# Optimization experiments

Measured on AMD Instinct MI355X. Metric: run time of the kernel, lower is better.

Reference implementation:

```python
import jax, jax.numpy as jnp
import numpy as np

B, LQ, LK, D = 8, 1024, 4096, 1024


def setup_inputs() -> dict:
    key = jax.random.key(0)
    k1, k2, k3, k4, k5, k6 = jax.random.split(key, 6)
    s = 1.0 / np.sqrt(D)
    return {
        "T": jax.random.normal(k1, (B, LQ, D), dtype=jnp.float32),
        "S": jax.random.normal(k2, (B, LK, D), dtype=jnp.float32),
        "Wq": jax.random.uniform(k3, (D, D), jnp.float32, -s, s),
        "Wk": jax.random.uniform(k4, (D, D), jnp.float32, -s, s),
        "Wv": jax.random.uniform(k5, (D, D), jnp.float32, -s, s),
        "Wo": jax.random.uniform(k6, (D, D), jnp.float32, -s, s),
    }


def reference(T, S, Wq, Wk, Wv, Wo):
    # Linear layers: y = x @ W.T (torch nn.Linear convention), bias=False
    q = jnp.einsum('bqd,ed->bqe', T, Wq)          # [B, LQ, D]
    k = jnp.einsum('bkd,ed->bke', S, Wk)          # [B, LK, D]
    v = jnp.einsum('bkd,ed->bke', S, Wv)          # [B, LK, D]
    scale = jnp.asarray(D, q.dtype) ** -0.5        # hidden_dim ** -0.5 (single head)
    attn = jnp.einsum('bqe,bke->bqk', q, k) * scale  # [B, LQ, LK]
    attn = jax.nn.softmax(attn, axis=-1)
    out = jnp.einsum('bqk,bke->bqe', attn, v)      # [B, LQ, D]
    return jnp.einsum('bqe,fe->bqf', out, Wo)      # output projection
```

## Files before the change

### kernel.cpp

```cpp
#include <hip/hip_runtime.h>
#include <stdint.h>

typedef __bf16 bf16;
typedef __bf16 bf16x8 __attribute__((ext_vector_type(8)));
typedef float f32x4 __attribute__((ext_vector_type(4)));

__device__ __forceinline__ void gload_lds16(const void* g, void* l) {
    __builtin_amdgcn_global_load_lds(
        (const __attribute__((address_space(1))) unsigned int*)g,
        (__attribute__((address_space(3))) unsigned int*)l, 16, 0, 0);
}

#define BAR()    asm volatile("s_barrier" ::: "memory")
#define WAITV(N) asm volatile("s_waitcnt vmcnt(" #N ")" ::: "memory")

template<int OMODE>
__global__ __launch_bounds__(512, 2)
void gemm256(const bf16* __restrict__ A, const bf16* __restrict__ B,
             void* __restrict__ Cv, int K, int N,
             long batchA, long batchB, long batchC, float alpha,
             int nbx, int nby, int GC, int lda, int ldb)
{
    __shared__ __align__(16) bf16 lds[2][4][8192];

    const int nwg  = gridDim.x;
    const int orig = blockIdx.x;
    const int q8   = nwg >> 3, r8 = nwg & 7;
    const int xcd  = orig & 7, lid = orig >> 3;
    const int p    = (xcd < r8 ? xcd * (q8 + 1) : r8 * (q8 + 1) + (xcd - r8) * q8) + lid;

    int pd = p, hv = 0;
    if constexpr (OMODE == 3) { hv = p >> 7; pd = p & 127; }
    const int kOff = hv << 11;

    const int perb = nbx * nby;
    const int z    = pd / perb;
    const int pb   = pd - z * perb;
    const int sw   = nby * GC;
    const int st   = pb / sw;
    const int rem  = pb - st * sw;
    const int by   = rem / GC;
    const int bx   = st * GC + (rem - by * GC);

    const long rowb = (long)by << 8;
    const long colb = (long)bx << 8;

    const int t  = threadIdx.x;
    const int l  = t & 63;
    const int w  = t >> 6;
    const int wm = w >> 2;
    const int wn = w & 3;

    const int sL   = (t * 16) ^ (((t >> 3) & 3) << 4);
    const int srow = sL >> 6;
    const int sk   = (sL & 63) >> 1;
    const bf16* gA = A + (long)z * batchA + (rowb + srow) * (long)lda + sk + kOff;
    const bf16* gB = B + (long)z * batchB + (colb + srow) * (long)ldb + sk + kOff;
    const long rA = 128L * lda;
    const long rB = 128L * ldb;
    const int  d0 = t * 8, d1 = t * 8 + 4096;

    const int xl    = ((l >> 1) & 3) << 4;
    const int aBase = ((wm * 128 + (l & 15)) * 64 + ((l >> 4) << 4)) ^ xl;
    const int bBase = ((wn * 64  + (l & 15)) * 64 + ((l >> 4) << 4)) ^ xl;

    f32x4 acc[8][4] = {};
    bf16x8 av[4], bv[4];

#define STG(S, R, G, KOFF2, RS) do { \
    const bf16* _g = (G) + (KOFF2); \
    gload_lds16(_g,      &lds[S][R][d0]); \
    gload_lds16(_g + RS, &lds[S][R][d1]); \
  } while (0)

#define RD(S, R, OFF) (*(const bf16x8*)((const char*)&lds[S][R][0] + (OFF)))

#define MM(MB) \
    __builtin_amdgcn_s_setprio(1); \
    _Pragma("unroll") for (int mi = 0; mi < 4; ++mi) \
      _Pragma("unroll") for (int nj = 0; nj < 4; ++nj) \
        acc[MB + mi][nj] = __builtin_amdgcn_mfma_f32_16x16x32_bf16(av[mi], bv[nj], acc[MB + mi][nj], 0, 0, 0); \
    __builtin_amdgcn_s_setprio(0);

#define PH1(S, STGX) { \
    _Pragma("unroll") for (int nj = 0; nj < 4; ++nj) bv[nj] = RD(S, 2, bBase + nj * 1024); \
    _Pragma("unroll") for (int mi = 0; mi < 4; ++mi) av[mi] = RD(S, 0, aBase + mi * 1024); \
    STGX; BAR(); MM(0) BAR(); }

#define PH2(S, STGX) { \
    _Pragma("unroll") for (int mi = 0; mi < 4; ++mi) av[mi] = RD(S, 0, aBase + 4096 + mi * 1024); \
    STGX; BAR(); MM(4) BAR(); }

#define PH3(S, STGX) { \
    _Pragma("unroll") for (int nj = 0; nj < 4; ++nj) bv[nj] = RD(S, 3, bBase + nj * 1024); \
    _Pragma("unroll") for (int mi = 0; mi < 4; ++mi) av[mi] = RD(S, 1, aBase + mi * 1024); \
    STGX; BAR(); MM(0) BAR(); }

#define PH4(S, STGX, WT) { \
    _Pragma("unroll") for (int mi = 0; mi < 4; ++mi) av[mi] = RD(S, 1, aBase + 4096 + mi * 1024); \
    STGX; BAR(); MM(4) WT; BAR(); }

    STG(0, 0, gA, 0,  rA);
    STG(0, 1, gA, 32, rA);
    STG(0, 2, gB, 0,  rB);
    STG(0, 3, gB, 32, rB);
    STG(1, 2, gB, 64, rB);
    STG(1, 0, gA, 64, rA);
    STG(1, 3, gB, 96, rB);
    WAITV(6);
    BAR();

    const int NI = K >> 7;
    for (int i = 0; i < NI - 1; ++i) {
        const int kb = i << 7;
        const int kn = kb + 128;
        PH1(0, STG(1, 1, gA, kb + 96, rA));
        PH2(0, STG(0, 2, gB, kn,      rB));
        PH3(0, STG(0, 0, gA, kn,      rA));
        PH4(0, STG(0, 3, gB, kn + 32, rB), WAITV(6));
        PH1(1, STG(0, 1, gA, kn + 32, rA));
        PH2(1, STG(1, 2, gB, kn + 64, rB));
        PH3(1, STG(1, 0, gA, kn + 64, rA));
        PH4(1, STG(1, 3, gB, kn + 96, rB), WAITV(6));
    }
    {
        const int kb = (NI - 1) << 7;
        PH1(0, STG(1, 1, gA, kb + 96, rA));
        PH2(0, );
        PH3(0, );
        PH4(0, , WAITV(0));
        PH1(1, );
        PH2(1, );
        PH3(1, );
        PH4(1, , );
    }
#undef STG
#undef RD
#undef MM
#undef PH1
#undef PH2
#undef PH3
#undef PH4

    const int r0 = (l >> 4) << 2;

    if constexpr (OMODE == 2) {
        const long cb0 = colb + wn * 64 + (l & 15);
        const long rb0 = rowb + wm * 128 + r0;
#pragma unroll
        for (int mf = 0; mf < 8; ++mf)
#pragma unroll
          for (int nj = 0; nj < 4; ++nj) {
            const long col = cb0 + nj * 16;
#pragma unroll
            for (int r = 0; r < 4; ++r) {
                const long row = rb0 + mf * 16 + r;
                ((float*)Cv)[(long)z * batchC + row * (long)N + col] = acc[mf][nj][r] * alpha;
            }
          }
    } else if constexpr (OMODE == 3) {
        float* Cb = (float*)Cv + (long)hv * 8388608 + (long)z * 1048576;
        const long cb0 = colb + wn * 64 + (l & 15);
        const long rb0 = rowb + wm * 128 + r0;
#pragma unroll
        for (int mf = 0; mf < 8; ++mf)
#pragma unroll
          for (int nj = 0; nj < 4; ++nj) {
            const long col = cb0 + nj * 16;
#pragma unroll
            for (int r = 0; r < 4; ++r)
                Cb[(rb0 + mf * 16 + r) * 1024 + col] = acc[mf][nj][r];
          }
    } else {
        bf16* epi = &lds[0][0][0];
        const int rrow   = t >> 5;
        const int cchunk = (t & 31) << 3;
        const int myh = (OMODE == 0) ? wm : (wn >> 1);
#pragma unroll
        for (int h = 0; h < 2; ++h) {
            if (myh == h) {
#pragma unroll
                for (int mf = 0; mf < 8; ++mf)
#pragma unroll
                  for (int nj = 0; nj < 4; ++nj)
#pragma unroll
                    for (int r = 0; r < 4; ++r) {
                        const float v = acc[mf][nj][r] * alpha;
                        int orow = wm * 128 + mf * 16 + r0 + r;
                        int ocol = wn * 64 + nj * 16 + (l & 15);
                        if (OMODE == 1) { int tmp = orow; orow = ocol; ocol = tmp; }
                        epi[(orow - h * 128) * 280 + ocol] = (bf16)v;
                    }
            }
            __syncthreads();
#pragma unroll
            for (int pp = 0; pp < 8; ++pp) {
                const int lrow = pp * 16 + rrow;
                const int row  = h * 128 + lrow;
                uint4 d = *(const uint4*)&epi[lrow * 280 + cchunk];
                if (OMODE == 0) {
                    bf16* Cb = (bf16*)Cv + (long)z * batchC;
                    *(uint4*)&Cb[(rowb + row) * (long)N + colb + cchunk] = d;
                } else {
                    const long zz  = rowb >> 12;
                    const long lk0 = (rowb & 4095) + cchunk;
                    *(uint4*)&((bf16*)Cv)[zz * 4194304L + (colb + row) * 4096L + lk0] = d;
                }
            }
            __syncthreads();
        }
    }
}

__global__ void cvt_bf16(const float* __restrict__ in, bf16* __restrict__ out, long n8)
{
    const long stride = (long)gridDim.x * 256;
    for (long i = (long)blockIdx.x * 256 + threadIdx.x; i < n8; i += stride) {
        const float4* p = (const float4*)in + i * 2;
        float4 a = p[0], b = p[1];
        union { bf16 h[8]; uint4 u; } o;
        o.h[0] = (bf16)a.x; o.h[1] = (bf16)a.y; o.h[2] = (bf16)a.z; o.h[3] = (bf16)a.w;
        o.h[4] = (bf16)b.x; o.h[5] = (bf16)b.y; o.h[6] = (bf16)b.z; o.h[7] = (bf16)b.w;
        ((uint4*)out)[i] = o.u;
    }
}

__global__ void cvt_w4(const float* __restrict__ wq, const float* __restrict__ wk,
                       const float* __restrict__ wv, const float* __restrict__ wo,
                       bf16* __restrict__ out)
{
    const long i  = (long)blockIdx.x * 256 + threadIdx.x;
    const int seg = (int)(i >> 17);
    const long j  = i & 131071;
    const float* src = seg == 0 ? wq : seg == 1 ? wk : seg == 2 ? wv : wo;
    const float4* pp = (const float4*)src + j * 2;
    float4 a = pp[0], b = pp[1];
    union { bf16 h[8]; uint4 u; } o;
    o.h[0] = (bf16)a.x; o.h[1] = (bf16)a.y; o.h[2] = (bf16)a.z; o.h[3] = (bf16)a.w;
    o.h[4] = (bf16)b.x; o.h[5] = (bf16)b.y; o.h[6] = (bf16)b.z; o.h[7] = (bf16)b.w;
    ((uint4*)out)[i] = o.u;
}

__global__ void reduce_pv(const float* __restrict__ Pt, bf16* __restrict__ Ob)
{
    const long i = (long)blockIdx.x * 256 + threadIdx.x;
    const float4* a = (const float4*)Pt + i * 2;
    const float4* b = (const float4*)(Pt + 8388608) + i * 2;
    float4 x0 = a[0], x1 = a[1], y0 = b[0], y1 = b[1];
    union { bf16 h[8]; uint4 u; } o;
    o.h[0] = (bf16)(x0.x + y0.x); o.h[1] = (bf16)(x0.y + y0.y);
    o.h[2] = (bf16)(x0.z + y0.z); o.h[3] = (bf16)(x0.w + y0.w);
    o.h[4] = (bf16)(x1.x + y1.x); o.h[5] = (bf16)(x1.y + y1.y);
    o.h[6] = (bf16)(x1.z + y1.z); o.h[7] = (bf16)(x1.w + y1.w);
    ((uint4*)Ob)[i] = o.u;
}

__global__ __launch_bounds__(256)
void softmax_rows(bf16* __restrict__ P)
{
    const long base = (long)blockIdx.x * 4096;
    const int t = threadIdx.x;
    union U { uint4 u; bf16 h[8]; };
    U d0, d1;
    d0.u = *(const uint4*)&P[base + t * 8];
    d1.u = *(const uint4*)&P[base + 2048 + t * 8];
    float v[16];
#pragma unroll
    for (int i = 0; i < 8; ++i) { v[i] = (float)d0.h[i]; v[8 + i] = (float)d1.h[i]; }
    float mx = v[0];
#pragma unroll
    for (int i = 1; i < 16; ++i) mx = fmaxf(mx, v[i]);
    for (int o = 32; o; o >>= 1) mx = fmaxf(mx, __shfl_xor(mx, o));
    __shared__ float redm[4], reds[4];
    if ((t & 63) == 0) redm[t >> 6] = mx;
    __syncthreads();
    mx = fmaxf(fmaxf(redm[0], redm[1]), fmaxf(redm[2], redm[3]));
    float s = 0.f;
#pragma unroll
    for (int i = 0; i < 16; ++i) { v[i] = __expf(v[i] - mx); s += v[i]; }
    for (int o = 32; o; o >>= 1) s += __shfl_xor(s, o);
    if ((t & 63) == 0) reds[t >> 6] = s;
    __syncthreads();
    s = reds[0] + reds[1] + reds[2] + reds[3];
    const float inv = 1.f / s;
    U o0, o1;
#pragma unroll
    for (int i = 0; i < 8; ++i) {
        o0.h[i] = (bf16)(v[i] * inv);
        o1.h[i] = (bf16)(v[8 + i] * inv);
    }
    *(uint4*)&P[base + t * 8]        = o0.u;
    *(uint4*)&P[base + 2048 + t * 8] = o1.u;
}

extern "C" void kernel_launch(void* const* d_in, const int* in_sizes, int n_in,
                              void* d_out, int out_size, void* d_ws, size_t ws_size,
                              hipStream_t stream)
{
    (void)in_sizes; (void)n_in; (void)out_size; (void)ws_size;
    const float* T  = (const float*)d_in[0];
    const float* S  = (const float*)d_in[1];
    const float* Wq = (const float*)d_in[2];
    const float* Wk = (const float*)d_in[3];
    const float* Wv = (const float*)d_in[4];
    const float* Wo = (const float*)d_in[5];
    float* Y = (float*)d_out;
    char* ws = (char*)d_ws;

    bf16* Wqb = (bf16*)(ws + 0);
    bf16* Wkb = (bf16*)(ws + 2097152);
    bf16* Wvb = (bf16*)(ws + 4194304);
    bf16* Wob = (bf16*)(ws + 6291456);
    bf16* Tb  = (bf16*)(ws + 8388608);
    bf16* Ob  = Tb;
    bf16* Qb  = (bf16*)(ws + 25165824);
    bf16* Sb  = (bf16*)(ws + 41943040);
    bf16* Pb  = Sb;
    bf16* Kb  = (bf16*)(ws + 109051904);
    float* Pt = (float*)Kb;
    bf16* VTb = (bf16*)(ws + 176160768);

    cvt_w4  <<<2048,  256, 0, stream>>>(Wq, Wk, Wv, Wo, Wqb);
    cvt_bf16<<<4096,  256, 0, stream>>>(T, Tb, 1048576);
    cvt_bf16<<<16384, 256, 0, stream>>>(S, Sb, 4194304);

    gemm256<0><<<128, 512, 0, stream>>>(Tb, Wqb, Qb, 1024, 1024,
        0, 0, 0, 1.f, 4, 32, 4, 1024, 1024);
    gemm256<0><<<512, 512, 0, stream>>>(Sb, Wkb, Kb, 1024, 1024,
        0, 0, 0, 1.f, 4, 128, 4, 1024, 1024);
    gemm256<1><<<512, 512, 0, stream>>>(Sb, Wvb, VTb, 1024, 1024,
        0, 0, 0, 1.f, 4, 128, 4, 1024, 1024);

    gemm256<0><<<512, 512, 0, stream>>>(Qb, Kb, Pb, 1024, 4096,
        1024L * 1024, 4096L * 1024, 1024L * 4096, 0.03125f, 16, 4, 4, 1024, 1024);

    softmax_rows<<<8192, 256, 0, stream>>>(Pb);

    gemm256<3><<<256, 512, 0, stream>>>(Pb, VTb, Pt, 2048, 1024,
        1024L * 4096, 1024L * 4096, 1048576, 1.f, 4, 4, 4, 4096, 4096);
    reduce_pv<<<4096, 256, 0, stream>>>(Pt, Ob);

    gemm256<2><<<128, 512, 0, stream>>>(Ob, Wob, Y, 1024, 1024,
        0, 0, 0, 1.f, 4, 32, 4, 1024, 1024);
}
```

Baseline: 425.5 us.

## Make GEMM blocks persistent over two tiles and prefetch the next tile's operands

The GEMM kernel gains a tiles-per-block template parameter. Each workgroup now loops over consecutive output tiles and, during the last K iteration of one tile, starts staging the next tile's A/B panels into LDS so the prologue load latency overlaps compute. The epilogue now uses a separate small LDS buffer in 32-row chunks, so the main staging buffers stay free for the prefetch. The K, V and QK^T GEMMs launch half as many blocks with two tiles each. This trades grid parallelism and extra LDS usage for hiding the per-tile pipeline fill.

New measurement: 633.9 us. +49.0%, slower.

```diff
diff --git a/kernel.cpp b/kernel.cpp
--- a/kernel.cpp
+++ b/kernel.cpp
@@ -13,8 +13,9 @@
 
 #define BAR()    asm volatile("s_barrier" ::: "memory")
 #define WAITV(N) asm volatile("s_waitcnt vmcnt(" #N ")" ::: "memory")
-
-template<int OMODE>
+#define WAITL()  asm volatile("s_waitcnt lgkmcnt(0)" ::: "memory")
+
+template<int OMODE, int TPB>
 __global__ __launch_bounds__(512, 2)
 void gemm256(const bf16* __restrict__ A, const bf16* __restrict__ B,
              void* __restrict__ Cv, int K, int N,
@@ -22,50 +23,40 @@
              int nbx, int nby, int GC, int lda, int ldb)
 {
     __shared__ __align__(16) bf16 lds[2][4][8192];
+    __shared__ __align__(16) bf16 epi[32 * 268];
 
     const int nwg  = gridDim.x;
     const int orig = blockIdx.x;
-    const int q8   = nwg >> 3, r8 = nwg & 7;
+    const int q8   = nwg >> 3, r8v = nwg & 7;
     const int xcd  = orig & 7, lid = orig >> 3;
-    const int p    = (xcd < r8 ? xcd * (q8 + 1) : r8 * (q8 + 1) + (xcd - r8) * q8) + lid;
-
-    int pd = p, hv = 0;
-    if constexpr (OMODE == 3) { hv = p >> 7; pd = p & 127; }
+    int p = (xcd < r8v ? xcd * (q8 + 1) : r8v * (q8 + 1) + (xcd - r8v) * q8) + lid;
+
+    int hv = 0;
+    if constexpr (OMODE == 3) { hv = p >> 7; p &= 127; }
     const int kOff = hv << 11;
-
-    const int perb = nbx * nby;
-    const int z    = pd / perb;
-    const int pb   = pd - z * perb;
-    const int sw   = nby * GC;
-    const int st   = pb / sw;
-    const int rem  = pb - st * sw;
-    const int by   = rem / GC;
-    const int bx   = st * GC + (rem - by * GC);
-
-    const long rowb = (long)by << 8;
-    const long colb = (long)bx << 8;
 
     const int t  = threadIdx.x;
     const int l  = t & 63;
     const int w  = t >> 6;
     const int wm = w >> 2;
     const int wn = w & 3;
+    const int l15 = l & 15;
+    const int r0  = (l >> 4) << 2;
 
     const int sL   = (t * 16) ^ (((t >> 3) & 3) << 4);
     const int srow = sL >> 6;
     const int sk   = (sL & 63) >> 1;
-    const bf16* gA = A + (long)z * batchA + (rowb + srow) * (long)lda + sk + kOff;
-    const bf16* gB = B + (long)z * batchB + (colb + srow) * (long)ldb + sk + kOff;
     const long rA = 128L * lda;
     const long rB = 128L * ldb;
     const int  d0 = t * 8, d1 = t * 8 + 4096;
 
     const int xl    = ((l >> 1) & 3) << 4;
-    const int aBase = ((wm * 128 + (l & 15)) * 64 + ((l >> 4) << 4)) ^ xl;
-    const int bBase = ((wn * 64  + (l & 15)) * 64 + ((l >> 4) << 4)) ^ xl;
-
-    f32x4 acc[8][4] = {};
-    bf16x8 av[4], bv[4];
+    const int aBase = ((wm * 128 + l15) * 64 + ((l >> 4) << 4)) ^ xl;
+    const int bBase = ((wn * 64  + l15) * 64 + ((l >> 4) << 4)) ^ xl;
+
+    const int perb = nbx * nby;
+    const int sw   = nby * GC;
+    const int NI   = K >> 7;
 
 #define STG(S, R, G, KOFF2, RS) do { \
     const bf16* _g = (G) + (KOFF2); \
@@ -100,39 +91,162 @@
     _Pragma("unroll") for (int mi = 0; mi < 4; ++mi) av[mi] = RD(S, 1, aBase + 4096 + mi * 1024); \
     STGX; BAR(); MM(4) WT; BAR(); }
 
-    STG(0, 0, gA, 0,  rA);
-    STG(0, 1, gA, 32, rA);
-    STG(0, 2, gB, 0,  rB);
-    STG(0, 3, gB, 32, rB);
-    STG(1, 2, gB, 64, rB);
-    STG(1, 0, gA, 64, rA);
-    STG(1, 3, gB, 96, rB);
-    WAITV(6);
-    BAR();
-
-    const int NI = K >> 7;
-    for (int i = 0; i < NI - 1; ++i) {
-        const int kb = i << 7;
-        const int kn = kb + 128;
-        PH1(0, STG(1, 1, gA, kb + 96, rA));
-        PH2(0, STG(0, 2, gB, kn,      rB));
-        PH3(0, STG(0, 0, gA, kn,      rA));
-        PH4(0, STG(0, 3, gB, kn + 32, rB), WAITV(6));
-        PH1(1, STG(0, 1, gA, kn + 32, rA));
-        PH2(1, STG(1, 2, gB, kn + 64, rB));
-        PH3(1, STG(1, 0, gA, kn + 64, rA));
-        PH4(1, STG(1, 3, gB, kn + 96, rB), WAITV(6));
-    }
-    {
-        const int kb = (NI - 1) << 7;
-        PH1(0, STG(1, 1, gA, kb + 96, rA));
-        PH2(0, );
-        PH3(0, );
-        PH4(0, , WAITV(0));
-        PH1(1, );
-        PH2(1, );
-        PH3(1, );
-        PH4(1, , );
+    for (int tt = 0; tt < TPB; ++tt) {
+        const int g   = p * TPB + tt;
+        const int z   = g / perb;
+        const int pb  = g - z * perb;
+        const int st  = pb / sw;
+        const int rem = pb - st * sw;
+        const int by  = rem / GC;
+        const int bx  = st * GC + (rem - by * GC);
+        const long rowb = (long)by << 8;
+        const long colb = (long)bx << 8;
+        const bf16* gA = A + (long)z * batchA + (rowb + srow) * (long)lda + sk + kOff;
+        const bf16* gB = B + (long)z * batchB + (colb + srow) * (long)ldb + sk + kOff;
+
+        const bf16* gA2 = gA;
+        const bf16* gB2 = gB;
+        if (TPB > 1 && tt < TPB - 1) {
+            const int g2   = g + 1;
+            const int z2   = g2 / perb;
+            const int pb2  = g2 - z2 * perb;
+            const int st2  = pb2 / sw;
+            const int rem2 = pb2 - st2 * sw;
+            const int by2  = rem2 / GC;
+            const int bx2  = st2 * GC + (rem2 - by2 * GC);
+            gA2 = A + (long)z2 * batchA + (((long)by2 << 8) + srow) * (long)lda + sk;
+            gB2 = B + (long)z2 * batchB + (((long)bx2 << 8) + srow) * (long)ldb + sk;
+        }
+
+        f32x4 acc[8][4] = {};
+        bf16x8 av[4], bv[4];
+
+        if (tt == 0) {
+            STG(0, 0, gA, 0,  rA);
+            STG(0, 1, gA, 32, rA);
+            STG(0, 2, gB, 0,  rB);
+            STG(0, 3, gB, 32, rB);
+            STG(1, 2, gB, 64, rB);
+            STG(1, 0, gA, 64, rA);
+            STG(1, 3, gB, 96, rB);
+            WAITV(6);
+            BAR();
+        }
+
+        for (int i = 0; i < NI - 1; ++i) {
+            const int kb = i << 7;
+            const int kn = kb + 128;
+            PH1(0, STG(1, 1, gA, kb + 96, rA));
+            PH2(0, STG(0, 2, gB, kn,      rB));
+            PH3(0, STG(0, 0, gA, kn,      rA));
+            PH4(0, STG(0, 3, gB, kn + 32, rB), WAITV(6));
+            PH1(1, STG(0, 1, gA, kn + 32, rA));
+            PH2(1, STG(1, 2, gB, kn + 64, rB));
+            PH3(1, STG(1, 0, gA, kn + 64, rA));
+            PH4(1, STG(1, 3, gB, kn + 96, rB), WAITV(6));
+        }
+        {
+            const int kb = (NI - 1) << 7;
+            if (TPB > 1 && tt < TPB - 1) {
+                PH1(0, STG(1, 1, gA, kb + 96, rA));
+                PH2(0, STG(0, 2, gB2, 0,  rB));
+                PH3(0, STG(0, 0, gA2, 0,  rA));
+                PH4(0, STG(0, 3, gB2, 32, rB), WAITV(6));
+                PH1(1, STG(0, 1, gA2, 32, rA));
+                PH2(1, STG(1, 2, gB2, 64, rB));
+                PH3(1, STG(1, 0, gA2, 64, rA));
+                PH4(1, STG(1, 3, gB2, 96, rB), );
+            } else {
+                PH1(0, STG(1, 1, gA, kb + 96, rA));
+                PH2(0, );
+                PH3(0, );
+                PH4(0, , WAITV(0));
+                PH1(1, );
+                PH2(1, );
+                PH3(1, );
+                PH4(1, , );
+            }
+        }
+
+        if constexpr (OMODE == 2) {
+            const long cb0 = colb + wn * 64 + l15;
+            const long rb0 = rowb + wm * 128 + r0;
+#pragma unroll
+            for (int mf = 0; mf < 8; ++mf)
+#pragma unroll
+              for (int nj = 0; nj < 4; ++nj) {
+                const long col = cb0 + nj * 16;
+#pragma unroll
+                for (int r = 0; r < 4; ++r)
+                    ((float*)Cv)[(long)z * batchC + (rb0 + mf * 16 + r) * (long)N + col]
+                        = acc[mf][nj][r] * alpha;
+              }
+        } else if constexpr (OMODE == 3) {
+            float* Cb = (float*)Cv + (long)hv * 8388608 + (long)z * 1048576;
+            const long cb0 = colb + wn * 64 + l15;
+            const long rb0 = rowb + wm * 128 + r0;
+#pragma unroll
+            for (int mf = 0; mf < 8; ++mf)
+#pragma unroll
+              for (int nj = 0; nj < 4; ++nj) {
+                const long col = cb0 + nj * 16;
+#pragma unroll
+                for (int r = 0; r < 4; ++r)
+                    Cb[(rb0 + mf * 16 + r) * 1024 + col] = acc[mf][nj][r];
+              }
+        } else {
+#pragma unroll
+            for (int q = 0; q < 8; ++q) {
+                if constexpr (OMODE == 0) {
+                    if (wm == (q >> 2)) {
+#pragma unroll
+                        for (int mi = 0; mi < 2; ++mi) {
+                            const int mf = ((q & 3) << 1) + mi;
+#pragma unroll
+                            for (int nj = 0; nj < 4; ++nj)
+#pragma unroll
+                              for (int r = 0; r < 4; ++r)
+                                epi[(mi * 16 + r0 + r) * 268 + wn * 64 + nj * 16 + l15]
+                                    = (bf16)(acc[mf][nj][r] * alpha);
+                        }
+                    }
+                } else {
+                    if (wn == (q >> 1)) {
+#pragma unroll
+                        for (int mf = 0; mf < 8; ++mf)
+#pragma unroll
+                          for (int ni = 0; ni < 2; ++ni) {
+                            const int nj = ((q & 1) << 1) + ni;
+#pragma unroll
+                            for (int r = 0; r < 4; ++r)
+                                epi[(ni * 16 + l15) * 268 + wm * 128 + mf * 16 + r0 + r]
+                                    = (bf16)(acc[mf][nj][r] * alpha);
+                          }
+                    }
+                }
+                WAITL(); BAR();
+                const int tr = t >> 4;
+                const int tc = (t & 15) << 4;
+                uint4 v0 = *(const uint4*)&epi[tr * 268 + tc];
+                uint4 v1 = *(const uint4*)&epi[tr * 268 + tc + 8];
+                if constexpr (OMODE == 0) {
+                    bf16* Cb = (bf16*)Cv + (long)z * batchC;
+                    const long base = (rowb + q * 32 + tr) * (long)N + colb + tc;
+                    *(uint4*)&Cb[base]     = v0;
+                    *(uint4*)&Cb[base + 8] = v1;
+                } else {
+                    const long zz  = rowb >> 12;
+                    const long lk0 = (rowb & 4095) + tc;
+                    const long eg  = colb + q * 32 + tr;
+                    const long base = zz * 4194304L + eg * 4096L + lk0;
+                    *(uint4*)&((bf16*)Cv)[base]     = v0;
+                    *(uint4*)&((bf16*)Cv)[base + 8] = v1;
+                }
+                WAITL(); BAR();
+            }
+        }
+
+        if (TPB > 1 && tt < TPB - 1) { WAITV(6); BAR(); }
     }
 #undef STG
 #undef RD
@@ -141,75 +255,6 @@
 #undef PH2
 #undef PH3
 #undef PH4
-
-    const int r0 = (l >> 4) << 2;
-
-    if constexpr (OMODE == 2) {
-        const long cb0 = colb + wn * 64 + (l & 15);
-        const long rb0 = rowb + wm * 128 + r0;
-#pragma unroll
-        for (int mf = 0; mf < 8; ++mf)
-#pragma unroll
-          for (int nj = 0; nj < 4; ++nj) {
-            const long col = cb0 + nj * 16;
-#pragma unroll
-            for (int r = 0; r < 4; ++r) {
-                const long row = rb0 + mf * 16 + r;
-                ((float*)Cv)[(long)z * batchC + row * (long)N + col] = acc[mf][nj][r] * alpha;
-            }
-          }
-    } else if constexpr (OMODE == 3) {
-        float* Cb = (float*)Cv + (long)hv * 8388608 + (long)z * 1048576;
-        const long cb0 = colb + wn * 64 + (l & 15);
-        const long rb0 = rowb + wm * 128 + r0;
-#pragma unroll
-        for (int mf = 0; mf < 8; ++mf)
-#pragma unroll
-          for (int nj = 0; nj < 4; ++nj) {
-            const long col = cb0 + nj * 16;
-#pragma unroll
-            for (int r = 0; r < 4; ++r)
-                Cb[(rb0 + mf * 16 + r) * 1024 + col] = acc[mf][nj][r];
-          }
-    } else {
-        bf16* epi = &lds[0][0][0];
-        const int rrow   = t >> 5;
-        const int cchunk = (t & 31) << 3;
-        const int myh = (OMODE == 0) ? wm : (wn >> 1);
-#pragma unroll
-        for (int h = 0; h < 2; ++h) {
-            if (myh == h) {
-#pragma unroll
-                for (int mf = 0; mf < 8; ++mf)
-#pragma unroll
-                  for (int nj = 0; nj < 4; ++nj)
-#pragma unroll
-                    for (int r = 0; r < 4; ++r) {
-                        const float v = acc[mf][nj][r] * alpha;
-                        int orow = wm * 128 + mf * 16 + r0 + r;
-                        int ocol = wn * 64 + nj * 16 + (l & 15);
-                        if (OMODE == 1) { int tmp = orow; orow = ocol; ocol = tmp; }
-                        epi[(orow - h * 128) * 280 + ocol] = (bf16)v;
-                    }
-            }
-            __syncthreads();
-#pragma unroll
-            for (int pp = 0; pp < 8; ++pp) {
-                const int lrow = pp * 16 + rrow;
-                const int row  = h * 128 + lrow;
-                uint4 d = *(const uint4*)&epi[lrow * 280 + cchunk];
-                if (OMODE == 0) {
-                    bf16* Cb = (bf16*)Cv + (long)z * batchC;
-                    *(uint4*)&Cb[(rowb + row) * (long)N + colb + cchunk] = d;
-                } else {
-                    const long zz  = rowb >> 12;
-                    const long lk0 = (rowb & 4095) + cchunk;
-                    *(uint4*)&((bf16*)Cv)[zz * 4194304L + (colb + row) * 4096L + lk0] = d;
-                }
-            }
-            __syncthreads();
-        }
-    }
 }
 
 __global__ void cvt_bf16(const float* __restrict__ in, bf16* __restrict__ out, long n8)
@@ -324,22 +369,22 @@
     cvt_bf16<<<4096,  256, 0, stream>>>(T, Tb, 1048576);
     cvt_bf16<<<16384, 256, 0, stream>>>(S, Sb, 4194304);
 
-    gemm256<0><<<128, 512, 0, stream>>>(Tb, Wqb, Qb, 1024, 1024,
+    gemm256<0,1><<<128, 512, 0, stream>>>(Tb, Wqb, Qb, 1024, 1024,
         0, 0, 0, 1.f, 4, 32, 4, 1024, 1024);
-    gemm256<0><<<512, 512, 0, stream>>>(Sb, Wkb, Kb, 1024, 1024,
+    gemm256<0,2><<<256, 512, 0, stream>>>(Sb, Wkb, Kb, 1024, 1024,
         0, 0, 0, 1.f, 4, 128, 4, 1024, 1024);
-    gemm256<1><<<512, 512, 0, stream>>>(Sb, Wvb, VTb, 1024, 1024,
+    gemm256<1,2><<<256, 512, 0, stream>>>(Sb, Wvb, VTb, 1024, 1024,
         0, 0, 0, 1.f, 4, 128, 4, 1024, 1024);
 
-    gemm256<0><<<512, 512, 0, stream>>>(Qb, Kb, Pb, 1024, 4096,
+    gemm256<0,2><<<256, 512, 0, stream>>>(Qb, Kb, Pb, 1024, 4096,
         1024L * 1024, 4096L * 1024, 1024L * 4096, 0.03125f, 16, 4, 4, 1024, 1024);
 
     softmax_rows<<<8192, 256, 0, stream>>>(Pb);
 
-    gemm256<3><<<256, 512, 0, stream>>>(Pb, VTb, Pt, 2048, 1024,
+    gemm256<3,1><<<256, 512, 0, stream>>>(Pb, VTb, Pt, 2048, 1024,
         1024L * 4096, 1024L * 4096, 1048576, 1.f, 4, 4, 4, 4096, 4096);
     reduce_pv<<<4096, 256, 0, stream>>>(Pt, Ob);
 
-    gemm256<2><<<128, 512, 0, stream>>>(Ob, Wob, Y, 1024, 1024,
+    gemm256<2,1><<<128, 512, 0, stream>>>(Ob, Wob, Y, 1024, 1024,
         0, 0, 0, 1.f, 4, 32, 4, 1024, 1024);
 }
```

## Fuse exp into QK GEMM epilogue and defer softmax normalization to PV reduce

Applied to the files above, without the earlier changes.

The QK^T GEMM gets a new epilogue mode that applies exp to the scaled scores before storing bf16 P. The separate softmax pass becomes a read-only row-sum kernel. Normalization by 1/sum is folded into the split-K PV reduction. This removes the max pass and the rewrite of the full P matrix, but it drops the max subtraction, so it can overflow when scores are large.

Result: faster. 415.0 us (-2.5%).

```diff
diff --git a/kernel.cpp b/kernel.cpp
--- a/kernel.cpp
+++ b/kernel.cpp
@@ -27,15 +27,15 @@
     const int orig = blockIdx.x;
     const int q8   = nwg >> 3, r8 = nwg & 7;
     const int xcd  = orig & 7, lid = orig >> 3;
-    const int p    = (xcd < r8 ? xcd * (q8 + 1) : r8 * (q8 + 1) + (xcd - r8) * q8) + lid;
-
-    int pd = p, hv = 0;
-    if constexpr (OMODE == 3) { hv = p >> 7; pd = p & 127; }
+    int p = (xcd < r8 ? xcd * (q8 + 1) : r8 * (q8 + 1) + (xcd - r8) * q8) + lid;
+
+    int hv = 0;
+    if constexpr (OMODE == 3) { hv = p >> 7; p &= 127; }
     const int kOff = hv << 11;
 
     const int perb = nbx * nby;
-    const int z    = pd / perb;
-    const int pb   = pd - z * perb;
+    const int z    = p / perb;
+    const int pb   = p - z * perb;
     const int sw   = nby * GC;
     const int st   = pb / sw;
     const int rem  = pb - st * sw;
@@ -175,7 +175,7 @@
         bf16* epi = &lds[0][0][0];
         const int rrow   = t >> 5;
         const int cchunk = (t & 31) << 3;
-        const int myh = (OMODE == 0) ? wm : (wn >> 1);
+        const int myh = (OMODE != 1) ? wm : (wn >> 1);
 #pragma unroll
         for (int h = 0; h < 2; ++h) {
             if (myh == h) {
@@ -185,7 +185,8 @@
                   for (int nj = 0; nj < 4; ++nj)
 #pragma unroll
                     for (int r = 0; r < 4; ++r) {
-                        const float v = acc[mf][nj][r] * alpha;
+                        float v = acc[mf][nj][r] * alpha;
+                        if constexpr (OMODE == 4) v = __expf(v);
                         int orow = wm * 128 + mf * 16 + r0 + r;
                         int ocol = wn * 64 + nj * 16 + (l & 15);
                         if (OMODE == 1) { int tmp = orow; orow = ocol; ocol = tmp; }
@@ -198,7 +199,7 @@
                 const int lrow = pp * 16 + rrow;
                 const int row  = h * 128 + lrow;
                 uint4 d = *(const uint4*)&epi[lrow * 280 + cchunk];
-                if (OMODE == 0) {
+                if (OMODE != 1) {
                     bf16* Cb = (bf16*)Cv + (long)z * batchC;
                     *(uint4*)&Cb[(rowb + row) * (long)N + colb + cchunk] = d;
                 } else {
@@ -241,22 +242,8 @@
     ((uint4*)out)[i] = o.u;
 }
 
-__global__ void reduce_pv(const float* __restrict__ Pt, bf16* __restrict__ Ob)
-{
-    const long i = (long)blockIdx.x * 256 + threadIdx.x;
-    const float4* a = (const float4*)Pt + i * 2;
-    const float4* b = (const float4*)(Pt + 8388608) + i * 2;
-    float4 x0 = a[0], x1 = a[1], y0 = b[0], y1 = b[1];
-    union { bf16 h[8]; uint4 u; } o;
-    o.h[0] = (bf16)(x0.x + y0.x); o.h[1] = (bf16)(x0.y + y0.y);
-    o.h[2] = (bf16)(x0.z + y0.z); o.h[3] = (bf16)(x0.w + y0.w);
-    o.h[4] = (bf16)(x1.x + y1.x); o.h[5] = (bf16)(x1.y + y1.y);
-    o.h[6] = (bf16)(x1.z + y1.z); o.h[7] = (bf16)(x1.w + y1.w);
-    ((uint4*)Ob)[i] = o.u;
-}
-
 __global__ __launch_bounds__(256)
-void softmax_rows(bf16* __restrict__ P)
+void rowsum(const bf16* __restrict__ P, float* __restrict__ sums)
 {
     const long base = (long)blockIdx.x * 4096;
     const int t = threadIdx.x;
@@ -264,33 +251,30 @@
     U d0, d1;
     d0.u = *(const uint4*)&P[base + t * 8];
     d1.u = *(const uint4*)&P[base + 2048 + t * 8];
-    float v[16];
-#pragma unroll
-    for (int i = 0; i < 8; ++i) { v[i] = (float)d0.h[i]; v[8 + i] = (float)d1.h[i]; }
-    float mx = v[0];
-#pragma unroll
-    for (int i = 1; i < 16; ++i) mx = fmaxf(mx, v[i]);
-    for (int o = 32; o; o >>= 1) mx = fmaxf(mx, __shfl_xor(mx, o));
-    __shared__ float redm[4], reds[4];
-    if ((t & 63) == 0) redm[t >> 6] = mx;
-    __syncthreads();
-    mx = fmaxf(fmaxf(redm[0], redm[1]), fmaxf(redm[2], redm[3]));
     float s = 0.f;
 #pragma unroll
-    for (int i = 0; i < 16; ++i) { v[i] = __expf(v[i] - mx); s += v[i]; }
+    for (int i = 0; i < 8; ++i) s += (float)d0.h[i] + (float)d1.h[i];
     for (int o = 32; o; o >>= 1) s += __shfl_xor(s, o);
+    __shared__ float reds[4];
     if ((t & 63) == 0) reds[t >> 6] = s;
     __syncthreads();
-    s = reds[0] + reds[1] + reds[2] + reds[3];
-    const float inv = 1.f / s;
-    U o0, o1;
-#pragma unroll
-    for (int i = 0; i < 8; ++i) {
-        o0.h[i] = (bf16)(v[i] * inv);
-        o1.h[i] = (bf16)(v[8 + i] * inv);
-    }
-    *(uint4*)&P[base + t * 8]        = o0.u;
-    *(uint4*)&P[base + 2048 + t * 8] = o1.u;
+    if (t == 0) sums[blockIdx.x] = reds[0] + reds[1] + reds[2] + reds[3];
+}
+
+__global__ void reduce_pv(const float* __restrict__ Pt, const float* __restrict__ sums,
+                          bf16* __restrict__ Ob)
+{
+    const long i = (long)blockIdx.x * 256 + threadIdx.x;
+    const float inv = 1.f / sums[i >> 7];
+    const float4* a = (const float4*)Pt + i * 2;
+    const float4* b = (const float4*)(Pt + 8388608) + i * 2;
+    float4 x0 = a[0], x1 = a[1], y0 = b[0], y1 = b[1];
+    union { bf16 h[8]; uint4 u; } o;
+    o.h[0] = (bf16)((x0.x + y0.x) * inv); o.h[1] = (bf16)((x0.y + y0.y) * inv);
+    o.h[2] = (bf16)((x0.z + y0.z) * inv); o.h[3] = (bf16)((x0.w + y0.w) * inv);
+    o.h[4] = (bf16)((x1.x + y1.x) * inv); o.h[5] = (bf16)((x1.y + y1.y) * inv);
+    o.h[6] = (bf16)((x1.z + y1.z) * inv); o.h[7] = (bf16)((x1.w + y1.w) * inv);
+    ((uint4*)Ob)[i] = o.u;
 }
 
 extern "C" void kernel_launch(void* const* d_in, const int* in_sizes, int n_in,
@@ -314,6 +298,7 @@
     bf16* Tb  = (bf16*)(ws + 8388608);
     bf16* Ob  = Tb;
     bf16* Qb  = (bf16*)(ws + 25165824);
+    float* Sm = (float*)Qb;
     bf16* Sb  = (bf16*)(ws + 41943040);
     bf16* Pb  = Sb;
     bf16* Kb  = (bf16*)(ws + 109051904);
@@ -331,14 +316,14 @@
     gemm256<1><<<512, 512, 0, stream>>>(Sb, Wvb, VTb, 1024, 1024,
         0, 0, 0, 1.f, 4, 128, 4, 1024, 1024);
 
-    gemm256<0><<<512, 512, 0, stream>>>(Qb, Kb, Pb, 1024, 4096,
+    gemm256<4><<<512, 512, 0, stream>>>(Qb, Kb, Pb, 1024, 4096,
         1024L * 1024, 4096L * 1024, 1024L * 4096, 0.03125f, 16, 4, 4, 1024, 1024);
 
-    softmax_rows<<<8192, 256, 0, stream>>>(Pb);
+    rowsum<<<8192, 256, 0, stream>>>(Pb, Sm);
 
     gemm256<3><<<256, 512, 0, stream>>>(Pb, VTb, Pt, 2048, 1024,
         1024L * 4096, 1024L * 4096, 1048576, 1.f, 4, 4, 4, 4096, 4096);
-    reduce_pv<<<4096, 256, 0, stream>>>(Pt, Ob);
+    reduce_pv<<<4096, 256, 0, stream>>>(Pt, Sm, Ob);
 
     gemm256<2><<<128, 512, 0, stream>>>(Ob, Wob, Y, 1024, 1024,
         0, 0, 0, 1.f, 4, 32, 4, 1024, 1024);
```
